# Optimization experiments

Measured on AMD Instinct MI355X. Metric: run time of the kernel, lower is better.

Reference implementation:

```python
import jax, jax.numpy as jnp
import numpy as np

D_MODEL = 192
D_INNER = 384          # expand(2) * d_model
HEADDIM = 12
NHEADS = 32            # d_inner // headdim
DSTATE = 16
NGROUPS = 1
CONV_DIM = D_INNER + 2 * NGROUPS * DSTATE          # 416
D_IN_PROJ = 2 * D_INNER + 2 * NGROUPS * DSTATE + NHEADS  # 832
LN_EPS = 1e-5


def silu(x):
    return x * jax.nn.sigmoid(x)


def depthwise_conv2d(x_nchw, w, b):
    # groups == channels depthwise conv, kernel 3, padding 1 (SAME)
    out = jax.lax.conv_general_dilated(
        x_nchw, w, window_strides=(1, 1), padding='SAME',
        feature_group_count=CONV_DIM,
        dimension_numbers=('NCHW', 'OIHW', 'NCHW'))
    return out + b[None, :, None, None]


def setup_inputs() -> dict:
    key = jax.random.key(0)
    ks = jax.random.split(key, 10)
    Bn, H, W = 4, 128, 128
    u = jax.random.normal(ks[0], (Bn, H, W, D_MODEL), jnp.float32)
    t = jax.random.normal(ks[1], (Bn, H, W, D_MODEL), jnp.float32)
    s_in = 1.0 / np.sqrt(D_MODEL)
    W_in = jax.random.normal(ks[2], (D_IN_PROJ, D_MODEL), jnp.float32) * s_in
    W_t_in = jax.random.normal(ks[3], (D_IN_PROJ, D_MODEL), jnp.float32) * s_in
    conv_w = jax.random.normal(ks[4], (CONV_DIM, 1, 3, 3), jnp.float32) * (1.0 / 3.0)
    conv_b = jnp.zeros((CONV_DIM,), jnp.float32)
    # dt_bias = inverse-softplus of dt sampled log-uniform in [dt_min, dt_max]
    dt0 = jnp.exp(jax.random.uniform(ks[5], (NHEADS,)) * (np.log(0.1) - np.log(0.001)) + np.log(0.001))
    dt_bias = dt0 + jnp.log(-jnp.expm1(-dt0))
    A_log = jnp.log(jax.random.uniform(ks[6], (NHEADS,), minval=1.0, maxval=16.0))
    D = jnp.ones((NHEADS,), jnp.float32)
    ln_gamma = jnp.ones((D_INNER,), jnp.float32)
    ln_beta = jnp.zeros((D_INNER,), jnp.float32)
    W_out = jax.random.normal(ks[7], (D_MODEL, D_INNER), jnp.float32) * (1.0 / np.sqrt(D_INNER))
    return dict(u=u, t=t, W_in=W_in, W_t_in=W_t_in, conv_w=conv_w, conv_b=conv_b,
                dt_bias=dt_bias, A_log=A_log, D=D, ln_gamma=ln_gamma, ln_beta=ln_beta,
                W_out=W_out)


def reference(u, t, W_in, W_t_in, conv_w, conv_b, dt_bias, A_log, D,
              ln_gamma, ln_beta, W_out):
    B0, H, W_, C0 = u.shape
    L = H * W_
    uu = u.reshape(B0, L, C0)
    tt = t.reshape(B0, L, C0)

    # in_proj on main branch: split into z, xBC, dt
    zxbcdt = uu @ W_in.T                                    # (B, L, 832)
    z = zxbcdt[..., :D_INNER]                               # (B, L, 384)
    xBC = zxbcdt[..., D_INNER:D_INNER + CONV_DIM]           # (B, L, 416)
    dt = zxbcdt[..., D_INNER + CONV_DIM:]                   # (B, L, 32)
    dt = jax.nn.softplus(dt + dt_bias)

    # t branch: only x1B1C1 part is ultimately used (C := C1)
    x1B1C1 = (tt @ W_t_in.T)[..., D_INNER:D_INNER + CONV_DIM]

    # depthwise 3x3 conv + silu on both branches
    xBC = xBC.reshape(B0, H, W_, CONV_DIM).transpose(0, 3, 1, 2)
    xBC = silu(depthwise_conv2d(xBC, conv_w, conv_b))
    xBC = xBC.transpose(0, 2, 3, 1).reshape(B0, L, CONV_DIM)

    x1B1C1 = x1B1C1.reshape(B0, H, W_, CONV_DIM).transpose(0, 3, 1, 2)
    x1B1C1 = silu(depthwise_conv2d(x1B1C1, conv_w, conv_b))
    x1B1C1 = x1B1C1.transpose(0, 2, 3, 1).reshape(B0, L, CONV_DIM)

    x = xBC[..., :D_INNER]                                  # V features (B, L, 384)
    Bk = xBC[..., D_INNER:D_INNER + NGROUPS * DSTATE]       # K (B, L, 16)
    Cq = x1B1C1[..., D_INNER + NGROUPS * DSTATE:]           # Q from t-branch (B, L, 16)

    A = -jnp.exp(A_log)                                     # (nheads,), negative

    # non-causal linear attention duality (ngroups == 1)
    V = x.reshape(B0, L, NHEADS, HEADDIM).transpose(0, 2, 1, 3)   # (B, h, L, d)
    dtT = dt.transpose(0, 2, 1)                                   # (B, h, L)
    dA = -(dtT[..., None] * A[None, :, None, None])               # ssd_positve_dA: positive
    V_scaled = V * dA
    KV = jnp.einsum('bln,bhld->bhnd', Bk, V_scaled)               # (B, h, 16, 12)
    y = jnp.einsum('bln,bhnd->bhld', Cq, KV) + V * D[None, :, None, None]
    y = y.transpose(0, 2, 1, 3).reshape(B0, L, D_INNER)

    # LayerNorm over d_inner
    mu = jnp.mean(y, axis=-1, keepdims=True)
    var = jnp.mean((y - mu) ** 2, axis=-1, keepdims=True)
    y = (y - mu) * jax.lax.rsqrt(var + LN_EPS) * ln_gamma + ln_beta

    y = y * z
    out = y @ W_out.T
    return out.reshape(B0, H, W_, C0)
```

## Files before the change

kernel.cpp:

```cpp
#include <hip/hip_runtime.h>
#include <hip/hip_bf16.h>
#include <math.h>


#define BN 4
#define HH 128
#define WWID 128
#define LTOK (HH*WWID)
#define NTOK (BN*LTOK)
#define DMODEL 192
#define DINNER 384
#define NH 32
#define HD 12
#define DST 16
#define CONVD 416
#define KVCHUNKS 64
#define PM 256
#define PBN 64
#define BSTR 200

typedef __hip_bfloat16 bf16;
typedef unsigned int uint32;
typedef unsigned short ushort16;
typedef __attribute__((ext_vector_type(8))) short bf16x8;
typedef __attribute__((ext_vector_type(4))) float f32x4;
typedef __attribute__((ext_vector_type(16))) float f32x16;

__device__ __forceinline__ float bflo(uint32 v){ return __uint_as_float((v & 0xffffu) << 16); }
__device__ __forceinline__ float bfhi(uint32 v){ return __uint_as_float(v & 0xffff0000u); }
__device__ __forceinline__ ushort16 f2bf(float f){
    __hip_bfloat16 h = __float2bfloat16(f);
    return *reinterpret_cast<const ushort16*>(&h);
}
__device__ __forceinline__ float softplusf(float x){
    return (x > 20.f) ? x : log1pf(expf(x));
}
__device__ __forceinline__ float siluf(float x){
    return x / (1.f + expf(-x));
}

union BFPK { short s[8]; bf16x8 v; };

__global__ __launch_bounds__(256) void k_prep(
    const float* __restrict__ Win, const float* __restrict__ Wout,
    const float* __restrict__ cw,
    bf16* __restrict__ Winbf, bf16* __restrict__ Woutbf, float* __restrict__ wtr)
{
    const int i = blockIdx.x*256 + threadIdx.x;
    if (i < 832*DMODEL)   Winbf[i]  = __float2bfloat16(Win[i]);
    if (i < DMODEL*DINNER) Woutbf[i] = __float2bfloat16(Wout[i]);
    if (i < CONVD*9) { const int c = i/9, k = i - c*9; wtr[k*420 + c] = cw[i]; }
}

__global__ __launch_bounds__(512) void k_proj_mfma(
    const float* __restrict__ u, const bf16* __restrict__ Wbf,
    const float* __restrict__ dt_b, const float* __restrict__ A_log,
    bf16* __restrict__ z_bf, bf16* __restrict__ xbc_pre, float* __restrict__ dA)
{
    __shared__ __align__(16) short S[2][PBN*BSTR];

    const int tid = threadIdx.x;
    const int m0 = blockIdx.x * PM;
    const int ntbase  = blockIdx.y * 7;
    const int ntiles  = blockIdx.y ? 6 : 7;
    const int wid = tid >> 6, lane = tid & 63;
    const int fr = lane & 31;
    const int hi = lane >> 5;

    bf16x8 a[12];
    {
        const float* arow = u + (size_t)(m0 + wid*32 + fr)*DMODEL;
        #pragma unroll
        for (int ks=0;ks<12;++ks) {
            const float4 a0 = *(const float4*)(arow + ks*16 + hi*8);
            const float4 a1 = *(const float4*)(arow + ks*16 + hi*8 + 4);
            BFPK pk;
            pk.s[0]=(short)f2bf(a0.x); pk.s[1]=(short)f2bf(a0.y);
            pk.s[2]=(short)f2bf(a0.z); pk.s[3]=(short)f2bf(a0.w);
            pk.s[4]=(short)f2bf(a1.x); pk.s[5]=(short)f2bf(a1.y);
            pk.s[6]=(short)f2bf(a1.z); pk.s[7]=(short)f2bf(a1.w);
            a[ks] = pk.v;
        }
    }

    const int srow = tid >> 3;
    const int sseg = tid & 7;
    uint4 r0, r1, r2;
    auto LOADB = [&](int nt) {
        const short* g = (const short*)Wbf + (size_t)(nt*PBN + srow)*DMODEL + sseg*24;
        r0 = *(const uint4*)g;
        r1 = *(const uint4*)(g + 8);
        r2 = *(const uint4*)(g + 16);
    };
    auto WRITEB = [&](int buf) {
        short* d = &S[buf][srow*BSTR + sseg*24];
        *(uint4*)d        = r0;
        *(uint4*)(d + 8)  = r1;
        *(uint4*)(d + 16) = r2;
    };

    LOADB(ntbase); WRITEB(0);
    LOADB(ntbase + 1);
    __syncthreads();

    for (int i = 0; i < ntiles; ++i) {
        const int nt  = ntbase + i;
        const int cur = i & 1;

        f32x16 acc0, acc1;
        #pragma unroll
        for (int q=0;q<16;++q) { acc0[q]=0.f; acc1[q]=0.f; }

        const short* Sb = &S[cur][0];
        #pragma unroll
        for (int ks=0;ks<12;++ks) {
            const bf16x8 b0 = *(const bf16x8*)&Sb[(fr     )*BSTR + ks*16 + hi*8];
            const bf16x8 b1 = *(const bf16x8*)&Sb[(32 + fr)*BSTR + ks*16 + hi*8];
            acc0 = __builtin_amdgcn_mfma_f32_32x32x16_bf16(a[ks], b0, acc0, 0, 0, 0);
            acc1 = __builtin_amdgcn_mfma_f32_32x32x16_bf16(a[ks], b1, acc1, 0, 0, 0);
        }

        #pragma unroll
        for (int ni=0;ni<2;++ni) {
            const f32x16& ac = ni ? acc1 : acc0;
            const int n0 = nt*64 + ni*32;
            const int n  = n0 + fr;
            if (n0 < DINNER) {
                #pragma unroll
                for (int r=0;r<16;++r) {
                    const int tok = m0 + wid*32 + (r&3) + 8*(r>>2) + 4*hi;
                    z_bf[(size_t)tok*DINNER + n] = __float2bfloat16(ac[r]);
                }
            } else if (n0 < 800) {
                #pragma unroll
                for (int r=0;r<16;++r) {
                    const int tok = m0 + wid*32 + (r&3) + 8*(r>>2) + 4*hi;
                    xbc_pre[(size_t)tok*CONVD + (n - DINNER)] = __float2bfloat16(ac[r]);
                }
            } else {
                const float db = dt_b[fr];
                const float al = expf(A_log[fr]);
                #pragma unroll
                for (int r=0;r<16;++r) {
                    const int tok = m0 + wid*32 + (r&3) + 8*(r>>2) + 4*hi;
                    const float dt = softplusf(ac[r] + db);
                    dA[(size_t)tok*NH + fr] = dt * al;
                }
            }
        }

        if (i + 1 < ntiles) {
            WRITEB(cur ^ 1);
            if (i + 2 < ntiles) LOADB(nt + 2);
        }
        __syncthreads();
    }
}

__global__ __launch_bounds__(256) void k_tproj(
    const float* __restrict__ t, const float* __restrict__ Wtin, float* __restrict__ cq_pre)
{
    __shared__ float ts[16][196];
    __shared__ float ws[16][196];
    const int tid = threadIdx.x;
    const int tok0 = blockIdx.x * 16;
    #pragma unroll
    for (int i = 0; i < 3; ++i) {
        const int flat = tid + 256*i;
        const int row = flat / 48, c = (flat % 48)*4;
        *(float4*)&ts[row][c] = *(const float4*)(t    + (size_t)(tok0+row)*DMODEL + c);
        *(float4*)&ws[row][c] = *(const float4*)(Wtin + (size_t)(784+row)*DMODEL + c);
    }
    __syncthreads();
    const int tt = tid >> 4, n = tid & 15;
    float s0=0.f,s1=0.f,s2=0.f,s3=0.f;
    #pragma unroll 4
    for (int k = 0; k < DMODEL; k += 4) {
        s0 = fmaf(ts[tt][k+0], ws[n][k+0], s0);
        s1 = fmaf(ts[tt][k+1], ws[n][k+1], s1);
        s2 = fmaf(ts[tt][k+2], ws[n][k+2], s2);
        s3 = fmaf(ts[tt][k+3], ws[n][k+3], s3);
    }
    cq_pre[(size_t)(tok0+tt)*DST + n] = (s0+s1)+(s2+s3);
}

__global__ __launch_bounds__(416) void k_conv416(
    const bf16* __restrict__ in, const float* __restrict__ wtr, const float* __restrict__ cb,
    bf16* __restrict__ out)
{
    __shared__ float ws[9*420];
    __shared__ float bs[416];
    const int tid = threadIdx.x;
    for (int i = tid; i < 9*420; i += 416) ws[i] = wtr[i];
    if (tid < 416) bs[tid] = cb[tid];
    __syncthreads();

    const int pl  = tid / 52;
    const int grp = tid - pl*52;
    const int c0  = grp*8;
    const int pix = blockIdx.x*8 + pl;
    const int hw  = pix & (LTOK-1);
    const int h = hw >> 7, w = hw & 127;
    const int bb = pix >> 14;

    float acc[8];
    {
        const float4 b0 = *(const float4*)&bs[c0];
        const float4 b1 = *(const float4*)&bs[c0+4];
        acc[0]=b0.x; acc[1]=b0.y; acc[2]=b0.z; acc[3]=b0.w;
        acc[4]=b1.x; acc[5]=b1.y; acc[6]=b1.z; acc[7]=b1.w;
    }

    #pragma unroll
    for (int dh=-1; dh<=1; ++dh) {
        const int hh = h + dh;
        if ((unsigned)hh >= (unsigned)HH) continue;
        #pragma unroll
        for (int dw=-1; dw<=1; ++dw) {
            const int w2 = w + dw;
            if ((unsigned)w2 >= (unsigned)WWID) continue;
            const int wi = (dh+1)*3 + (dw+1);
            const size_t off = ((size_t)((bb<<14) + (hh<<7) + w2))*CONVD + c0;
            const uint4 v = *(const uint4*)((const ushort16*)in + off);
            const float4 w0 = *(const float4*)&ws[wi*420 + c0];
            const float4 w1 = *(const float4*)&ws[wi*420 + c0 + 4];
            acc[0] = fmaf(bflo(v.x), w0.x, acc[0]);
            acc[1] = fmaf(bfhi(v.x), w0.y, acc[1]);
            acc[2] = fmaf(bflo(v.y), w0.z, acc[2]);
            acc[3] = fmaf(bfhi(v.y), w0.w, acc[3]);
            acc[4] = fmaf(bflo(v.z), w1.x, acc[4]);
            acc[5] = fmaf(bfhi(v.z), w1.y, acc[5]);
            acc[6] = fmaf(bflo(v.w), w1.z, acc[6]);
            acc[7] = fmaf(bfhi(v.w), w1.w, acc[7]);
        }
    }

    uint4 o;
    o.x = ((uint32)f2bf(siluf(acc[1])) << 16) | (uint32)f2bf(siluf(acc[0]));
    o.y = ((uint32)f2bf(siluf(acc[3])) << 16) | (uint32)f2bf(siluf(acc[2]));
    o.z = ((uint32)f2bf(siluf(acc[5])) << 16) | (uint32)f2bf(siluf(acc[4]));
    o.w = ((uint32)f2bf(siluf(acc[7])) << 16) | (uint32)f2bf(siluf(acc[6]));
    *(uint4*)((ushort16*)out + (size_t)pix*CONVD + c0) = o;
}

__global__ __launch_bounds__(256) void k_conv16(
    const float* __restrict__ in, const float* __restrict__ cw, const float* __restrict__ cb,
    float* __restrict__ out)
{
    const int idx = blockIdx.x*256 + threadIdx.x;
    const int cc = idx & 15;
    const int pix = idx >> 4;
    const int hw = pix & (LTOK-1);
    const int h = hw >> 7, w = hw & 127;
    const int bb = pix >> 14;
    const int c = 400 + cc;

    float wg[9];
    #pragma unroll
    for (int k=0;k<9;++k) wg[k] = cw[c*9+k];
    float a = cb[c];
    #pragma unroll
    for (int dh=-1; dh<=1; ++dh) {
        const int hh = h + dh;
        if ((unsigned)hh >= (unsigned)HH) continue;
        #pragma unroll
        for (int dw=-1; dw<=1; ++dw) {
            const int w2 = w + dw;
            if ((unsigned)w2 >= (unsigned)WWID) continue;
            a = fmaf(in[((size_t)((bb<<14)+(hh<<7)+w2))*16 + cc], wg[(dh+1)*3 + (dw+1)], a);
        }
    }
    out[(size_t)pix*16 + cc] = siluf(a);
}

__global__ __launch_bounds__(512) void k_kv(
    const bf16* __restrict__ xbc_post, const float* __restrict__ dA,
    float* __restrict__ partial)
{
    __shared__ short vsb[16][408];
    __shared__ float das[16][32];
    const int tid = threadIdx.x;
    const int b = blockIdx.y;
    const int n = tid & 15;
    const int g = tid >> 4;

    float acc[12];
    #pragma unroll
    for (int j=0;j<12;++j) acc[j]=0.f;

    const int l0base = b*LTOK + blockIdx.x*256;

    for (int it = 0; it < 16; ++it) {
        const int l0 = l0base + it*16;
        for (int i = tid; i < 16*200; i += 512) {
            const int tok = i / 200;
            const int c2 = i - tok*200;
            const uint32 v = *(const uint32*)((const ushort16*)xbc_post
                                + (size_t)(l0+tok)*CONVD + c2*2);
            *(uint32*)&vsb[tok][c2*2] = v;
        }
        {
            const int tok = tid >> 5, h = tid & 31;
            das[tok][h] = dA[(size_t)(l0+tok)*NH + h];
        }
        __syncthreads();

        #pragma unroll
        for (int tok = 0; tok < 16; ++tok) {
            const uint32 bkraw = (uint32)(ushort16)vsb[tok][DINNER + n];
            const float s = __uint_as_float(bkraw << 16) * das[tok][g];
            const uint32* vp = (const uint32*)&vsb[tok][g*12];
            const uint32 w0 = vp[0], w1 = vp[1], w2 = vp[2];
            acc[0]  = fmaf(s, bflo(w0), acc[0]);
            acc[1]  = fmaf(s, bfhi(w0), acc[1]);
            acc[2]  = fmaf(s, bflo(w1), acc[2]);
            acc[3]  = fmaf(s, bfhi(w1), acc[3]);
            acc[4]  = fmaf(s, bflo(w2), acc[4]);
            acc[5]  = fmaf(s, bfhi(w2), acc[5]);
            const uint32* vq = (const uint32*)&vsb[tok][g*12 + 6];
            const uint32 w3 = vq[0], w4 = vq[1], w5 = vq[2];
            acc[6]  = fmaf(s, bflo(w3), acc[6]);
            acc[7]  = fmaf(s, bfhi(w3), acc[7]);
            acc[8]  = fmaf(s, bflo(w4), acc[8]);
            acc[9]  = fmaf(s, bfhi(w4), acc[9]);
            acc[10] = fmaf(s, bflo(w5), acc[10]);
            acc[11] = fmaf(s, bfhi(w5), acc[11]);
        }
        __syncthreads();
    }

    float* dst = partial + ((size_t)(b*KVCHUNKS + blockIdx.x))*6144 + (size_t)tid*12;
    #pragma unroll
    for (int j4=0;j4<3;++j4)
        *(float4*)(dst + j4*4) = make_float4(acc[j4*4], acc[j4*4+1], acc[j4*4+2], acc[j4*4+3]);
}

__global__ __launch_bounds__(256) void k_kvred(
    const float* __restrict__ partial, float* __restrict__ kv)
{
    const int idx = blockIdx.x*256 + threadIdx.x;
    const int b = idx / 6144;
    const int flat = idx - b*6144;
    const float* p = partial + (size_t)(b*KVCHUNKS)*6144 + flat;
    float s = 0.f;
    #pragma unroll 4
    for (int c = 0; c < KVCHUNKS; ++c) s += p[(size_t)c*6144];
    kv[idx] = s;
}

__global__ __launch_bounds__(256) void k_ynorm(
    const bf16* __restrict__ xbc_post, const float* __restrict__ cq_post,
    const bf16* __restrict__ z_bf, const float* __restrict__ kv,
    const float* __restrict__ Dv, const float* __restrict__ ln_g, const float* __restrict__ ln_b,
    bf16* __restrict__ yz)
{
    __shared__ float kvs[NH*DST*HD];
    __shared__ float ys[16][386];
    __shared__ float cqs[16][16];
    const int tid = threadIdx.x;
    const int token0 = blockIdx.x * 16;
    const int b = token0 >> 14;

    for (int i = tid; i < NH*DST*HD; i += 256) {
        const int n = i / DINNER;
        const int hd = i - n*DINNER;
        const int h = hd / HD;
        const int d = hd - h*HD;
        kvs[i] = kv[((size_t)(b*NH + h)*DST + n)*HD + d];
    }
    {
        const int tt = tid >> 4, n2 = tid & 15;
        cqs[tt][n2] = cq_post[(size_t)(token0+tt)*DST + n2];
    }
    __syncthreads();

    #pragma unroll
    for (int jj=0; jj<12; ++jj) {
        const int flat = jj*256 + tid;
        const int tt = flat / 192;
        const int p  = flat - tt*192;
        const int hd = p*2;
        const int h = hd / HD;
        const int l = token0 + tt;
        const uint32 v = *(const uint32*)((const ushort16*)xbc_post + (size_t)l*CONVD + hd);
        const float dv = Dv[h];
        float a0 = bflo(v) * dv;
        float a1 = bfhi(v) * dv;
        #pragma unroll
        for (int n=0;n<16;++n) {
            const float c = cqs[tt][n];
            const float2 kk = *(const float2*)&kvs[n*DINNER + hd];
            a0 = fmaf(c, kk.x, a0);
            a1 = fmaf(c, kk.y, a1);
        }
        *(float2*)&ys[tt][hd] = make_float2(a0, a1);
    }
    __syncthreads();

    const int wave = tid >> 6, lane = tid & 63;
    #pragma unroll
    for (int i=0;i<4;++i) {
        const int tt = wave*4 + i;
        const int l = token0 + tt;
        float v[6]; float s=0.f, s2=0.f;
        #pragma unroll
        for (int k=0;k<6;++k){ const float x = ys[tt][k*64+lane]; v[k]=x; s+=x; s2=fmaf(x,x,s2); }
        #pragma unroll
        for (int off=32; off>0; off>>=1){ s += __shfl_xor(s,off,64); s2 += __shfl_xor(s2,off,64); }
        const float mu = s*(1.f/384.f);
        const float var = s2*(1.f/384.f) - mu*mu;
        const float rs = rsqrtf(var + 1e-5f);
        #pragma unroll
        for (int k=0;k<6;++k){
            const int idx = k*64+lane;
            const float yn = (v[k]-mu)*rs*ln_g[idx] + ln_b[idx];
            const uint32 zb = (uint32)(*((const ushort16*)z_bf + (size_t)l*DINNER + idx));
            const float zv = __uint_as_float(zb << 16);
            yz[(size_t)l*DINNER + idx] = __float2bfloat16(yn*zv);
        }
    }
}

__global__ __launch_bounds__(256) void k_out_mfma(
    const bf16* __restrict__ yz, const bf16* __restrict__ Wbf, float* __restrict__ out)
{
    __shared__ __align__(16) short As[2][128*40];
    __shared__ __align__(16) short Bs[2][192*40];

    const int tid = threadIdx.x;
    const int m0 = blockIdx.x * 128;
    const int wid = tid >> 6, lane = tid & 63;
    const int wm = wid >> 1, wn = wid & 1;
    const int fr = lane & 15, fq = lane >> 4;

    const int arow = tid >> 1, ahalf = tid & 1;
    auto stageA = [&](int ks, int buf) {
        const short* g = (const short*)yz + (size_t)(m0 + arow)*DINNER + ks*32 + ahalf*16;
        const uint4 v0 = *(const uint4*)g;
        const uint4 v1 = *(const uint4*)(g + 8);
        short* d = &As[buf][arow*40 + ahalf*16];
        *(uint4*)d = v0;
        *(uint4*)(d + 8) = v1;
    };
    auto stageB = [&](int ks, int buf) {
        #pragma unroll
        for (int i = 0; i < 3; ++i) {
            const int flat = tid + 256*i;
            const int row = flat >> 2, q = flat & 3;
            const uint4 v = *(const uint4*)((const short*)Wbf + (size_t)row*DINNER + ks*32 + q*8);
            *(uint4*)&Bs[buf][row*40 + q*8] = v;
        }
    };

    f32x4 acc[4][6];
    #pragma unroll
    for (int mi=0;mi<4;++mi)
        #pragma unroll
        for (int ni=0;ni<6;++ni) acc[mi][ni] = (f32x4){0.f,0.f,0.f,0.f};

    stageA(0, 0); stageB(0, 0);
    __syncthreads();

    const int aoff = (wm*64 + fr)*40 + fq*8;
    const int boff = (wn*96 + fr)*40 + fq*8;

    #pragma unroll
    for (int ks = 0; ks < 12; ++ks) {
        const int cur = ks & 1;
        if (ks < 11) { stageA(ks+1, cur^1); stageB(ks+1, cur^1); }
        bf16x8 a[4], b[6];
        #pragma unroll
        for (int mi=0;mi<4;++mi) a[mi] = *(const bf16x8*)(&As[cur][aoff + mi*640]);
        #pragma unroll
        for (int ni=0;ni<6;++ni) b[ni] = *(const bf16x8*)(&Bs[cur][boff + ni*640]);
        #pragma unroll
        for (int mi=0;mi<4;++mi)
            #pragma unroll
            for (int ni=0;ni<6;++ni)
                acc[mi][ni] = __builtin_amdgcn_mfma_f32_16x16x32_bf16(a[mi], b[ni], acc[mi][ni], 0, 0, 0);
        __syncthreads();
    }

    #pragma unroll
    for (int mi=0;mi<4;++mi) {
        #pragma unroll
        for (int j=0;j<4;++j) {
            const int tok = m0 + wm*64 + mi*16 + fq*4 + j;
            #pragma unroll
            for (int ni=0;ni<6;++ni) {
                const int n = wn*96 + ni*16 + fr;
                out[(size_t)tok*DMODEL + n] = acc[mi][ni][j];
            }
        }
    }
}

extern "C" void kernel_launch(void* const* d_in, const int* in_sizes, int n_in,
                              void* d_out, int out_size, void* d_ws, size_t ws_size,
                              hipStream_t stream)
{
    const float* u      = (const float*)d_in[0];
    const float* t      = (const float*)d_in[1];
    const float* Win    = (const float*)d_in[2];
    const float* Wtin   = (const float*)d_in[3];
    const float* conv_w = (const float*)d_in[4];
    const float* conv_b = (const float*)d_in[5];
    const float* dt_b   = (const float*)d_in[6];
    const float* A_log  = (const float*)d_in[7];
    const float* Dv     = (const float*)d_in[8];
    const float* ln_g   = (const float*)d_in[9];
    const float* ln_bt  = (const float*)d_in[10];
    const float* W_out  = (const float*)d_in[11];
    float* out = (float*)d_out;

    char* p = (char*)d_ws;
    bf16* z_bf     = (bf16*)p;  p += (size_t)NTOK*DINNER*2;
    bf16* xbc_pre  = (bf16*)p;  p += (size_t)NTOK*CONVD*2;
    bf16* xbc_post = (bf16*)p;  p += (size_t)NTOK*CONVD*2;
    float* cq_pre  = (float*)p; p += (size_t)NTOK*DST*4;
    float* cq_post = (float*)p; p += (size_t)NTOK*DST*4;
    float* dA      = (float*)p; p += (size_t)NTOK*NH*4;
    bf16* yz       = (bf16*)p;  p += (size_t)NTOK*DINNER*2;
    float* kv      = (float*)p; p += (size_t)BN*NH*DST*HD*4;
    bf16* Win_bf   = (bf16*)p;  p += (size_t)832*DMODEL*2;
    bf16* Wout_bf  = (bf16*)p;  p += (size_t)DMODEL*DINNER*2;
    float* wtr     = (float*)p; p += (size_t)9*420*4;

    float* kv_part = (float*)xbc_pre;

    k_prep<<<624, 256, 0, stream>>>(Win, W_out, conv_w, Win_bf, Wout_bf, wtr);
    k_proj_mfma<<<dim3(NTOK/PM, 2), 512, 0, stream>>>(u, Win_bf, dt_b, A_log, z_bf, xbc_pre, dA);
    k_tproj<<<NTOK/16, 256, 0, stream>>>(t, Wtin, cq_pre);
    k_conv416<<<NTOK/8, 416, 0, stream>>>(xbc_pre, wtr, conv_b, xbc_post);
    k_conv16<<<NTOK*16/256, 256, 0, stream>>>(cq_pre, conv_w, conv_b, cq_post);
    k_kv<<<dim3(KVCHUNKS, BN), 512, 0, stream>>>(xbc_post, dA, kv_part);
    k_kvred<<<BN*6144/256, 256, 0, stream>>>(kv_part, kv);
    k_ynorm<<<NTOK/16, 256, 0, stream>>>(xbc_post, cq_post, z_bf, kv,
                                         Dv, ln_g, ln_bt, yz);
    k_out_mfma<<<512, 256, 0, stream>>>(yz, Wout_bf, out);
}
```

Baseline: 332.6 us.

## Compute Cq·KV in ynorm with bf16 MFMA and register-resident LayerNorm

The y = Cq·KV + D·V step in k_ynorm now runs on 16x16x32 bf16 MFMA instead of scalar FMAs. KV is split into bf16 hi and lo parts packed along K, so a single MFMA per 16-column tile keeps near-fp32 accuracy for KV. Cq is now bf16. LayerNorm statistics are reduced in registers with 16-lane shuffles, removing the ys shared-memory round trip, and each block handles 64 tokens instead of 16. The k_conv16 output becomes bf16 to feed the MFMA directly. The cost is precision loss on Cq and uncoalesced 2-byte per-lane loads and stores of xbc_post, z and yz.

```diff
diff --git a/kernel.cpp b/kernel.cpp
--- a/kernel.cpp
+++ b/kernel.cpp
@@ -31,6 +31,9 @@
 __device__ __forceinline__ ushort16 f2bf(float f){
     __hip_bfloat16 h = __float2bfloat16(f);
     return *reinterpret_cast<const ushort16*>(&h);
+}
+__device__ __forceinline__ float ldbf(const bf16* p){
+    return __uint_as_float(((uint32)(*(const ushort16*)p)) << 16);
 }
 __device__ __forceinline__ float softplusf(float x){
     return (x > 20.f) ? x : log1pf(expf(x));
@@ -245,7 +248,7 @@
 
 __global__ __launch_bounds__(256) void k_conv16(
     const float* __restrict__ in, const float* __restrict__ cw, const float* __restrict__ cb,
-    float* __restrict__ out)
+    bf16* __restrict__ out)
 {
     const int idx = blockIdx.x*256 + threadIdx.x;
     const int cc = idx & 15;
@@ -270,7 +273,7 @@
             a = fmaf(in[((size_t)((bb<<14)+(hh<<7)+w2))*16 + cc], wg[(dh+1)*3 + (dw+1)], a);
         }
     }
-    out[(size_t)pix*16 + cc] = siluf(a);
+    out[(size_t)pix*16 + cc] = __float2bfloat16(siluf(a));
 }
 
 __global__ __launch_bounds__(512) void k_kv(
@@ -349,74 +352,103 @@
 }
 
 __global__ __launch_bounds__(256) void k_ynorm(
-    const bf16* __restrict__ xbc_post, const float* __restrict__ cq_post,
+    const bf16* __restrict__ xbc_post, const bf16* __restrict__ cq_bf,
     const bf16* __restrict__ z_bf, const float* __restrict__ kv,
     const float* __restrict__ Dv, const float* __restrict__ ln_g, const float* __restrict__ ln_b,
     bf16* __restrict__ yz)
 {
-    __shared__ float kvs[NH*DST*HD];
-    __shared__ float ys[16][386];
-    __shared__ float cqs[16][16];
+    __shared__ __align__(16) short kvb[24*64*8];
+    __shared__ float gs[DINNER], bs2[DINNER], ds[DINNER];
     const int tid = threadIdx.x;
-    const int token0 = blockIdx.x * 16;
+    const int token0 = blockIdx.x * 64;
     const int b = token0 >> 14;
-
-    for (int i = tid; i < NH*DST*HD; i += 256) {
-        const int n = i / DINNER;
-        const int hd = i - n*DINNER;
-        const int h = hd / HD;
-        const int d = hd - h*HD;
-        kvs[i] = kv[((size_t)(b*NH + h)*DST + n)*HD + d];
-    }
-    {
-        const int tt = tid >> 4, n2 = tid & 15;
-        cqs[tt][n2] = cq_post[(size_t)(token0+tt)*DST + n2];
+    const float* kvB = kv + (size_t)b*6144;
+
+    for (int i = tid; i < DINNER; i += 256) {
+        gs[i]  = ln_g[i];
+        bs2[i] = ln_b[i];
+        ds[i]  = Dv[i/HD];
+    }
+    #pragma unroll
+    for (int it = 0; it < 6; ++it) {
+        const int f = tid + 256*it;
+        const int t = f >> 6, l = f & 63;
+        const int q = l >> 4;
+        const int nb = (q & 1)*8;
+        const int hd = t*16 + (l & 15);
+        const int h = hd/HD, d = hd - h*HD;
+        const float* src = kvB + (size_t)h*192 + d;
+        BFPK pk;
+        #pragma unroll
+        for (int i = 0; i < 8; ++i) {
+            const float v = src[(size_t)(nb+i)*12];
+            if (q < 2) {
+                pk.s[i] = (short)f2bf(v);
+            } else {
+                const uint32 hb = (uint32)(ushort16)f2bf(v);
+                pk.s[i] = (short)f2bf(v - __uint_as_float(hb << 16));
+            }
+        }
+        *(bf16x8*)&kvb[(size_t)f*8] = pk.v;
     }
     __syncthreads();
 
-    #pragma unroll
-    for (int jj=0; jj<12; ++jj) {
-        const int flat = jj*256 + tid;
-        const int tt = flat / 192;
-        const int p  = flat - tt*192;
-        const int hd = p*2;
-        const int h = hd / HD;
-        const int l = token0 + tt;
-        const uint32 v = *(const uint32*)((const ushort16*)xbc_post + (size_t)l*CONVD + hd);
-        const float dv = Dv[h];
-        float a0 = bflo(v) * dv;
-        float a1 = bfhi(v) * dv;
-        #pragma unroll
-        for (int n=0;n<16;++n) {
-            const float c = cqs[tt][n];
-            const float2 kk = *(const float2*)&kvs[n*DINNER + hd];
-            a0 = fmaf(c, kk.x, a0);
-            a1 = fmaf(c, kk.y, a1);
-        }
-        *(float2*)&ys[tt][hd] = make_float2(a0, a1);
-    }
-    __syncthreads();
-
-    const int wave = tid >> 6, lane = tid & 63;
-    #pragma unroll
-    for (int i=0;i<4;++i) {
-        const int tt = wave*4 + i;
-        const int l = token0 + tt;
-        float v[6]; float s=0.f, s2=0.f;
-        #pragma unroll
-        for (int k=0;k<6;++k){ const float x = ys[tt][k*64+lane]; v[k]=x; s+=x; s2=fmaf(x,x,s2); }
-        #pragma unroll
-        for (int off=32; off>0; off>>=1){ s += __shfl_xor(s,off,64); s2 += __shfl_xor(s2,off,64); }
-        const float mu = s*(1.f/384.f);
-        const float var = s2*(1.f/384.f) - mu*mu;
-        const float rs = rsqrtf(var + 1e-5f);
-        #pragma unroll
-        for (int k=0;k<6;++k){
-            const int idx = k*64+lane;
-            const float yn = (v[k]-mu)*rs*ln_g[idx] + ln_b[idx];
-            const uint32 zb = (uint32)(*((const ushort16*)z_bf + (size_t)l*DINNER + idx));
-            const float zv = __uint_as_float(zb << 16);
-            yz[(size_t)l*DINNER + idx] = __float2bfloat16(yn*zv);
+    const int wid = tid >> 6, lane = tid & 63;
+    const int fr = lane & 15, fq = lane >> 4;
+    const int tokA = token0 + wid*16;
+
+    const bf16x8 cqf = *(const bf16x8*)((const short*)cq_bf + (size_t)(tokA+fr)*DST + (fq&1)*8);
+
+    f32x4 acc[24];
+    #pragma unroll
+    for (int t = 0; t < 24; ++t) {
+        const bf16x8 bfv = *(const bf16x8*)&kvb[(t*64 + lane)*8];
+        f32x4 z4 = (f32x4){0.f,0.f,0.f,0.f};
+        acc[t] = __builtin_amdgcn_mfma_f32_16x16x32_bf16(cqf, bfv, z4, 0, 0, 0);
+    }
+
+    const int tokj0 = tokA + fq*4;
+    float s[4]  = {0.f,0.f,0.f,0.f};
+    float s2[4] = {0.f,0.f,0.f,0.f};
+    #pragma unroll
+    for (int t = 0; t < 24; ++t) {
+        const int hd = t*16 + fr;
+        const float dvh = ds[hd];
+        #pragma unroll
+        for (int j = 0; j < 4; ++j) {
+            const float vv = ldbf(xbc_post + (size_t)(tokj0+j)*CONVD + hd);
+            const float y = fmaf(vv, dvh, acc[t][j]);
+            acc[t][j] = y;
+            s[j] += y;
+            s2[j] = fmaf(y, y, s2[j]);
+        }
+    }
+    #pragma unroll
+    for (int j = 0; j < 4; ++j) {
+        #pragma unroll
+        for (int off = 8; off > 0; off >>= 1) {
+            s[j]  += __shfl_xor(s[j],  off, 16);
+            s2[j] += __shfl_xor(s2[j], off, 16);
+        }
+    }
+    float mu[4], rs[4];
+    #pragma unroll
+    for (int j = 0; j < 4; ++j) {
+        mu[j] = s[j] * (1.f/384.f);
+        const float var = s2[j]*(1.f/384.f) - mu[j]*mu[j];
+        rs[j] = rsqrtf(var + 1e-5f);
+    }
+
+    #pragma unroll
+    for (int t = 0; t < 24; ++t) {
+        const int hd = t*16 + fr;
+        const float g = gs[hd], be = bs2[hd];
+        #pragma unroll
+        for (int j = 0; j < 4; ++j) {
+            const int tok = tokj0 + j;
+            const float yn = fmaf((acc[t][j] - mu[j])*rs[j], g, be);
+            const float zv = ldbf(z_bf + (size_t)tok*DINNER + hd);
+            yz[(size_t)tok*DINNER + hd] = __float2bfloat16(yn*zv);
         }
     }
 }
@@ -518,7 +550,7 @@
     bf16* xbc_pre  = (bf16*)p;  p += (size_t)NTOK*CONVD*2;
     bf16* xbc_post = (bf16*)p;  p += (size_t)NTOK*CONVD*2;
     float* cq_pre  = (float*)p; p += (size_t)NTOK*DST*4;
-    float* cq_post = (float*)p; p += (size_t)NTOK*DST*4;
+    bf16* cq_bf    = (bf16*)p;  p += (size_t)NTOK*DST*2;
     float* dA      = (float*)p; p += (size_t)NTOK*NH*4;
     bf16* yz       = (bf16*)p;  p += (size_t)NTOK*DINNER*2;
     float* kv      = (float*)p; p += (size_t)BN*NH*DST*HD*4;
@@ -532,10 +564,10 @@
     k_proj_mfma<<<dim3(NTOK/PM, 2), 512, 0, stream>>>(u, Win_bf, dt_b, A_log, z_bf, xbc_pre, dA);
     k_tproj<<<NTOK/16, 256, 0, stream>>>(t, Wtin, cq_pre);
     k_conv416<<<NTOK/8, 416, 0, stream>>>(xbc_pre, wtr, conv_b, xbc_post);
-    k_conv16<<<NTOK*16/256, 256, 0, stream>>>(cq_pre, conv_w, conv_b, cq_post);
+    k_conv16<<<NTOK*16/256, 256, 0, stream>>>(cq_pre, conv_w, conv_b, cq_bf);
     k_kv<<<dim3(KVCHUNKS, BN), 512, 0, stream>>>(xbc_post, dA, kv_part);
     k_kvred<<<BN*6144/256, 256, 0, stream>>>(kv_part, kv);
-    k_ynorm<<<NTOK/16, 256, 0, stream>>>(xbc_post, cq_post, z_bf, kv,
+    k_ynorm<<<NTOK/64, 256, 0, stream>>>(xbc_post, cq_bf, z_bf, kv,
                                          Dv, ln_g, ln_bt, yz);
     k_out_mfma<<<512, 256, 0, stream>>>(yz, Wout_bf, out);
 }
```

New measurement: 310.9 us. -6.5%, faster.
